# Optimization experiments

Measured on AMD Instinct MI355X. Metric: run time of the kernel, lower is better.

## Reference

```python
import jax, jax.numpy as jnp
import numpy as np

B, S, E, H, MAXLEN = 2, 2048, 1024, 16, 2048


def _level_indices(seq_len: int, base: int = 2) -> np.ndarray:
    """Vectorized version of get_level_index_weak over the full (target, source) grid.
    indices[t, s] = min(level, 2) for s < t, else 0. Runs in O(log S) passes."""
    tt = np.broadcast_to(np.arange(seq_len)[:, None], (seq_len, seq_len)).astype(np.int64).copy()
    ss = np.broadcast_to(np.arange(seq_len)[None, :], (seq_len, seq_len)).astype(np.int64).copy()
    res = np.zeros((seq_len, seq_len), np.int64)
    done = ~(ss < tt)  # only source < target positions get a level; rest stay 0
    while not done.all():
        l = np.floor(np.log2(np.maximum(tt, 1).astype(np.float64))).astype(np.int64)
        v = (np.int64(1) << l)
        hit = (~done) & (ss < v)
        res[hit] = l[hit] + 1
        done |= hit
        step = ~done
        tt[step] -= v[step]
        ss[step] -= v[step]
    return np.minimum(res, 2).astype(np.int32)


def setup_inputs() -> dict:
    key = jax.random.key(0)
    ks = jax.random.split(key, 10)
    sc = 0.02
    return {
        "x": jax.random.normal(ks[0], (B, S, E), dtype=jnp.float32),
        "attention_mask": jax.random.randint(ks[1], (B, S), 0, 2, dtype=jnp.int32),
        "level_indices": jnp.asarray(_level_indices(S, 2)),
        "Wq": jax.random.normal(ks[2], (E, E), dtype=jnp.float32) * sc,
        "bq": jnp.zeros((E,), jnp.float32),
        "Wk": jax.random.normal(ks[3], (E, E), dtype=jnp.float32) * sc,
        "bk": jnp.zeros((E,), jnp.float32),
        "Wv": jax.random.normal(ks[4], (E, E), dtype=jnp.float32) * sc,
        "bv": jnp.zeros((E,), jnp.float32),
        "hier": jax.random.normal(ks[5], (MAXLEN, H, 3), dtype=jnp.float32),
        "Wo": jax.random.normal(ks[6], (E, E), dtype=jnp.float32) * sc,
        "bo": jnp.zeros((E,), jnp.float32),
    }


def reference(x, attention_mask, level_indices, Wq, bq, Wk, bk, Wv, bv, hier, Wo, bo):
    b, s, e = x.shape
    h = hier.shape[1]
    dh = e // h
    # q/k are computed by the original module but never used; kept for fidelity (zero grads).
    q = x @ Wq.T + bq
    k = x @ Wk.T + bk
    v = (x @ Wv.T + bv).reshape(b, s, h, dh).transpose(0, 2, 1, 3)  # [B,H,S,Dh]
    lev = level_indices[:s, :s]  # [S,S] int, values in {0,1,2}
    # Faithful torch.gather semantics: weights[b,h,i,j] = hier[b, h, lev[i,j]]
    w3 = hier[:b]                      # [B,H,3]
    weights = w3[:, :, lev]            # [B,H,S,S]
    decay = jnp.power(jnp.float32(0.5), lev.astype(x.dtype))  # [S,S]
    weights = weights * decay
    weights = weights / (jnp.sum(weights, axis=-1, keepdims=True) + 1e-8)
    weights = jnp.where(attention_mask[:, None, None, :] == 0, jnp.float32(0.0), weights)
    out = jnp.einsum('bhij,bhjd->bhid', weights, v)  # [B,H,S,Dh]
    out = out.transpose(0, 2, 1, 3).reshape(b, s, e)
    return out @ Wo.T + bo
```

## Files before the change

### kernel.cpp

```cpp
#include <hip/hip_runtime.h>
#include <cstdint>
#include <cstddef>

constexpr int Sn = 2048;
constexpr int En = 1024;
constexpr int Bn = 2;
constexpr int Hn = 16;
constexpr int CHUNK = 32;
constexpr int NCH = Sn / CHUNK;
constexpr int Mtot = Bn * Sn;
constexpr int GCH = Mtot / CHUNK;

typedef __bf16 bf16x8 __attribute__((ext_vector_type(8)));
typedef float  f32x4  __attribute__((ext_vector_type(4)));

#define GLOBAL_AS(p) ((const __attribute__((address_space(1))) void*)(p))
#define LDS_AS(p)    ((__attribute__((address_space(3))) void*)(p))

__device__ __forceinline__ unsigned short f2bf(float f) {
    union { float f; uint32_t u; } v; v.f = f;
    const uint32_t u = v.u;
    return (unsigned short)((u + 0x7fffu + ((u >> 16) & 1u)) >> 16);
}
__device__ __forceinline__ float bf2f(unsigned short s) {
    union { uint32_t u; float f; } v; v.u = (uint32_t)s << 16; return v.f;
}

constexpr int XN = Bn * Sn * En;
constexpr int WN = En * En;

__global__ __launch_bounds__(256)
void cast3(const float* __restrict__ x, const float* __restrict__ Wv,
           const float* __restrict__ Wo, unsigned short* __restrict__ xb,
           unsigned short* __restrict__ Wvb, unsigned short* __restrict__ Wob)
{
    const int i = (blockIdx.x * 256 + threadIdx.x) * 4;
    const float* src; unsigned short* dst; int off;
    if (i < XN)           { src = x;  dst = xb;  off = i; }
    else if (i < XN + WN) { src = Wv; dst = Wvb; off = i - XN; }
    else                  { src = Wo; dst = Wob; off = i - XN - WN; }
    const float4 v = *(const float4*)(src + off);
    ushort4 o;
    o.x = f2bf(v.x); o.y = f2bf(v.y); o.z = f2bf(v.z); o.w = f2bf(v.w);
    *(ushort4*)(dst + off) = o;
}

template<bool APPLY_MASK, bool OUT_BF16, bool FUSE_CSUM>
__global__ __launch_bounds__(256, 4)
void gemm64(const unsigned short* __restrict__ A, const unsigned short* __restrict__ Bw,
            const float* __restrict__ bias, const int* __restrict__ mask,
            void* __restrict__ Cv, float* __restrict__ csum, int M, int N, int K)
{
    __shared__ __align__(16) unsigned short As[64 * 64];
    __shared__ __align__(16) unsigned short Bs[64 * 64];

    const int tid  = threadIdx.x;
    const int lane = tid & 63;
    const int wv   = tid >> 6;
    const int wr   = wv >> 1;
    const int wc   = wv & 1;
    const int id   = blockIdx.y * 16 + blockIdx.x;
    const int xcd  = id & 7;
    const int slot = id >> 3;
    const int by   = xcd * 8 + (slot >> 4);
    const int bx   = slot & 15;
    const int bm   = by * 64;
    const int bn   = bx * 64;
    const int m16  = lane & 15;
    const int kq   = lane >> 4;

    f32x4 acc[2][2] = {};

    const unsigned short* gA = A  + (size_t)(bm + 16 * wv + m16) * K + kq * 8;
    const unsigned short* gB = Bw + (size_t)(bn + 16 * wv + m16) * K + kq * 8;
    unsigned short* lA0 = &As[(wv * 2 + 0) * 512];
    unsigned short* lA1 = &As[(wv * 2 + 1) * 512];
    unsigned short* lB0 = &Bs[(wv * 2 + 0) * 512];
    unsigned short* lB1 = &Bs[(wv * 2 + 1) * 512];

#pragma unroll 1
    for (int k0 = 0; k0 < K; k0 += 64) {
        __syncthreads();
        __builtin_amdgcn_global_load_lds(GLOBAL_AS(gA + k0),      LDS_AS(lA0), 16, 0, 0);
        __builtin_amdgcn_global_load_lds(GLOBAL_AS(gA + k0 + 32), LDS_AS(lA1), 16, 0, 0);
        __builtin_amdgcn_global_load_lds(GLOBAL_AS(gB + k0),      LDS_AS(lB0), 16, 0, 0);
        __builtin_amdgcn_global_load_lds(GLOBAL_AS(gB + k0 + 32), LDS_AS(lB1), 16, 0, 0);
        __syncthreads();

        bf16x8 af[2][2], bfr[2][2];
#pragma unroll
        for (int i = 0; i < 2; ++i)
#pragma unroll
            for (int kh = 0; kh < 2; ++kh) {
                af[i][kh]  = *(const bf16x8*)&As[((2 * wr + i) * 2 + kh) * 512 + lane * 8];
                bfr[i][kh] = *(const bf16x8*)&Bs[((2 * wc + i) * 2 + kh) * 512 + lane * 8];
            }
#pragma unroll
        for (int kh = 0; kh < 2; ++kh)
#pragma unroll
            for (int i = 0; i < 2; ++i)
#pragma unroll
                for (int j = 0; j < 2; ++j)
                    acc[i][j] = __builtin_amdgcn_mfma_f32_16x16x32_bf16(af[i][kh], bfr[j][kh], acc[i][j], 0, 0, 0);
    }

    float colsum[2] = {0.0f, 0.0f};
#pragma unroll
    for (int i = 0; i < 2; ++i) {
        const int r0 = bm + wr * 32 + i * 16 + kq * 4;
#pragma unroll
        for (int j = 0; j < 2; ++j) {
            const int c0 = bn + wc * 32 + j * 16 + m16;
            const float bcol = bias[c0];
#pragma unroll
            for (int r = 0; r < 4; ++r) {
                const int row = r0 + r;
                float val = acc[i][j][r] + bcol;
                if (APPLY_MASK) val = (mask[row] == 0) ? 0.0f : val;
                if (FUSE_CSUM) colsum[j] += val;
                if (OUT_BF16)
                    ((unsigned short*)Cv)[(size_t)row * N + c0] = f2bf(val);
                else
                    ((float*)Cv)[(size_t)row * N + c0] = val;
            }
        }
    }

    if (FUSE_CSUM) {
        const int gc = 2 * by + wr;
#pragma unroll
        for (int j = 0; j < 2; ++j) {
            float s = colsum[j];
            s += __shfl_xor(s, 16, 64);
            s += __shfl_xor(s, 32, 64);
            if (kq == 0)
                csum[(size_t)gc * En + bn + wc * 32 + j * 16 + m16] = s;
        }
    }
}

__global__ __launch_bounds__(256)
void combine(const unsigned short* __restrict__ vm, const float* __restrict__ csum,
             const float* __restrict__ hier, unsigned short* __restrict__ opre)
{
    const int e = blockIdx.x * 256 + threadIdx.x;
    const int c = blockIdx.y;
    const int b = blockIdx.z;
    const int h = e >> 6;

    const float w0 = hier[((size_t)b * Hn + h) * 3 + 0];
    const float w1 = hier[((size_t)b * Hn + h) * 3 + 1] * 0.5f;
    const float w2 = hier[((size_t)b * Hn + h) * 3 + 2] * 0.25f;

    float run = 0.0f, T = 0.0f;
    const int g0 = b * NCH;
    for (int c2 = 0; c2 < NCH; ++c2) {
        const float v = csum[(size_t)(g0 + c2) * En + e];
        if (c2 < c) run += v;
        T += v;
    }

    float prev = 0.0f;
    const size_t base = ((size_t)b * Sn + c * CHUNK) * En + e;

    for (int t = 0; t < CHUNK; ++t) {
        const int i = c * CHUNK + t;
        const float cur = bf2f(vm[base + (size_t)t * En]);
        float num, Z;
        if (i & 1) {
            num = w2 * (run - prev) + w1 * prev + w0 * (T - run);
            Z = (float)(i - 1) * w2 + w1 + (float)(Sn - i) * w0 + 1e-8f;
        } else {
            num = w2 * run + w0 * (T - run);
            Z = (float)i * w2 + (float)(Sn - i) * w0 + 1e-8f;
        }
        opre[base + (size_t)t * En] = f2bf(num / Z);
        run += cur;
        prev = cur;
    }
}

extern "C" void kernel_launch(void* const* d_in, const int* in_sizes, int n_in,
                              void* d_out, int out_size, void* d_ws, size_t ws_size,
                              hipStream_t stream)
{
    const float* x    = (const float*)d_in[0];
    const int*   mask = (const int*)d_in[1];
    const float* Wv   = (const float*)d_in[7];
    const float* bv   = (const float*)d_in[8];
    const float* hier = (const float*)d_in[9];
    const float* Wo   = (const float*)d_in[10];
    const float* bo   = (const float*)d_in[11];
    float* out = (float*)d_out;

    const int M = Mtot, N = En, K = En;

    char* ws = (char*)d_ws;
    unsigned short* xb    = (unsigned short*)ws;  ws += (size_t)M * K * 2;
    unsigned short* Wvb   = (unsigned short*)ws;  ws += (size_t)N * K * 2;
    unsigned short* Wob   = (unsigned short*)ws;  ws += (size_t)N * K * 2;
    unsigned short* vmb   = (unsigned short*)ws;  ws += (size_t)M * N * 2;
    float*          csum  = (float*)ws;           ws += (size_t)GCH * En * 4;
    unsigned short* opreb = (unsigned short*)ws;  ws += (size_t)M * N * 2;

    dim3 threads(256);

    cast3<<<dim3((XN + 2 * WN) / 1024), threads, 0, stream>>>(x, Wv, Wo, xb, Wvb, Wob);

    dim3 gemm_grid(16, 64);

    gemm64<true, true, true><<<gemm_grid, threads, 0, stream>>>(xb, Wvb, bv, mask, vmb, csum, M, N, K);
    combine<<<dim3(En / 256, NCH, Bn), threads, 0, stream>>>(vmb, csum, hier, opreb);
    gemm64<false, false, false><<<gemm_grid, threads, 0, stream>>>(opreb, Wob, bo, nullptr, out, nullptr, M, N, K);
}
```

Before: 181.4 us.

## Pre-swizzle operands into MFMA fragment layout and drop LDS staging in GEMMs

The cast and combine kernels now write bf16 operands in a blocked layout that matches the MFMA 16x32 fragment order. The GEMM then loads fragments straight from global memory into registers with no LDS or barriers. The block tile grows to 128x64 with 4x2 accumulators per wave, and CHUNK doubles to 64 to match the new row tiling of the column sums. The cost is that operand reuse now relies on L2/cache instead of LDS, and the combine kernel's writes become scattered.

```diff
diff --git a/kernel.cpp b/kernel.cpp
--- a/kernel.cpp
+++ b/kernel.cpp
@@ -6,16 +6,14 @@
 constexpr int En = 1024;
 constexpr int Bn = 2;
 constexpr int Hn = 16;
-constexpr int CHUNK = 32;
+constexpr int CHUNK = 64;
 constexpr int NCH = Sn / CHUNK;
 constexpr int Mtot = Bn * Sn;
 constexpr int GCH = Mtot / CHUNK;
+constexpr int KB = En / 32;
 
 typedef __bf16 bf16x8 __attribute__((ext_vector_type(8)));
 typedef float  f32x4  __attribute__((ext_vector_type(4)));
-
-#define GLOBAL_AS(p) ((const __attribute__((address_space(1))) void*)(p))
-#define LDS_AS(p)    ((__attribute__((address_space(3))) void*)(p))
 
 __device__ __forceinline__ unsigned short f2bf(float f) {
     union { float f; uint32_t u; } v; v.f = f;
@@ -24,6 +22,11 @@
 }
 __device__ __forceinline__ float bf2f(unsigned short s) {
     union { uint32_t u; float f; } v; v.u = (uint32_t)s << 16; return v.f;
+}
+
+__device__ __forceinline__ size_t swz_idx(int r, int c, int kb ) {
+    const int blk = (r >> 4) * kb + (c >> 5);
+    return (size_t)blk * 512 + (((r & 15) + (((c >> 3) & 3) << 4)) << 3) + (c & 7);
 }
 
 constexpr int XN = Bn * Sn * En;
@@ -42,18 +45,16 @@
     const float4 v = *(const float4*)(src + off);
     ushort4 o;
     o.x = f2bf(v.x); o.y = f2bf(v.y); o.z = f2bf(v.z); o.w = f2bf(v.w);
-    *(ushort4*)(dst + off) = o;
+    const int r = off >> 10, c = off & 1023;
+    *(ushort4*)(dst + swz_idx(r, c, KB)) = o;
 }
 
 template<bool APPLY_MASK, bool OUT_BF16, bool FUSE_CSUM>
-__global__ __launch_bounds__(256, 4)
-void gemm64(const unsigned short* __restrict__ A, const unsigned short* __restrict__ Bw,
-            const float* __restrict__ bias, const int* __restrict__ mask,
-            void* __restrict__ Cv, float* __restrict__ csum, int M, int N, int K)
-{
-    __shared__ __align__(16) unsigned short As[64 * 64];
-    __shared__ __align__(16) unsigned short Bs[64 * 64];
-
+__global__ __launch_bounds__(256)
+void gemm_flat(const unsigned short* __restrict__ A, const unsigned short* __restrict__ Bw,
+               const float* __restrict__ bias, const int* __restrict__ mask,
+               void* __restrict__ Cv, float* __restrict__ csum)
+{
     const int tid  = threadIdx.x;
     const int lane = tid & 63;
     const int wv   = tid >> 6;
@@ -62,52 +63,42 @@
     const int id   = blockIdx.y * 16 + blockIdx.x;
     const int xcd  = id & 7;
     const int slot = id >> 3;
-    const int by   = xcd * 8 + (slot >> 4);
+    const int by   = xcd * 4 + (slot >> 4);
     const int bx   = slot & 15;
-    const int bm   = by * 64;
+    const int bm   = by * 128;
     const int bn   = bx * 64;
     const int m16  = lane & 15;
     const int kq   = lane >> 4;
 
-    f32x4 acc[2][2] = {};
-
-    const unsigned short* gA = A  + (size_t)(bm + 16 * wv + m16) * K + kq * 8;
-    const unsigned short* gB = Bw + (size_t)(bn + 16 * wv + m16) * K + kq * 8;
-    unsigned short* lA0 = &As[(wv * 2 + 0) * 512];
-    unsigned short* lA1 = &As[(wv * 2 + 1) * 512];
-    unsigned short* lB0 = &Bs[(wv * 2 + 0) * 512];
-    unsigned short* lB1 = &Bs[(wv * 2 + 1) * 512];
-
-#pragma unroll 1
-    for (int k0 = 0; k0 < K; k0 += 64) {
-        __syncthreads();
-        __builtin_amdgcn_global_load_lds(GLOBAL_AS(gA + k0),      LDS_AS(lA0), 16, 0, 0);
-        __builtin_amdgcn_global_load_lds(GLOBAL_AS(gA + k0 + 32), LDS_AS(lA1), 16, 0, 0);
-        __builtin_amdgcn_global_load_lds(GLOBAL_AS(gB + k0),      LDS_AS(lB0), 16, 0, 0);
-        __builtin_amdgcn_global_load_lds(GLOBAL_AS(gB + k0 + 32), LDS_AS(lB1), 16, 0, 0);
-        __syncthreads();
-
-        bf16x8 af[2][2], bfr[2][2];
-#pragma unroll
-        for (int i = 0; i < 2; ++i)
-#pragma unroll
-            for (int kh = 0; kh < 2; ++kh) {
-                af[i][kh]  = *(const bf16x8*)&As[((2 * wr + i) * 2 + kh) * 512 + lane * 8];
-                bfr[i][kh] = *(const bf16x8*)&Bs[((2 * wc + i) * 2 + kh) * 512 + lane * 8];
-            }
-#pragma unroll
-        for (int kh = 0; kh < 2; ++kh)
-#pragma unroll
-            for (int i = 0; i < 2; ++i)
-#pragma unroll
-                for (int j = 0; j < 2; ++j)
-                    acc[i][j] = __builtin_amdgcn_mfma_f32_16x16x32_bf16(af[i][kh], bfr[j][kh], acc[i][j], 0, 0, 0);
+    f32x4 acc[4][2] = {};
+
+    const int rb = by * 8 + wr * 4;
+    const int cb = bx * 4 + wc * 2;
+    const unsigned short* aBase = A  + (size_t)rb * KB * 512 + lane * 8;
+    const unsigned short* bBase = Bw + (size_t)cb * KB * 512 + lane * 8;
+
+#pragma unroll 4
+    for (int kc = 0; kc < KB; ++kc) {
+        bf16x8 af0 = *(const bf16x8*)(aBase + (size_t)(0 * KB + kc) * 512);
+        bf16x8 af1 = *(const bf16x8*)(aBase + (size_t)(1 * KB + kc) * 512);
+        bf16x8 af2 = *(const bf16x8*)(aBase + (size_t)(2 * KB + kc) * 512);
+        bf16x8 af3 = *(const bf16x8*)(aBase + (size_t)(3 * KB + kc) * 512);
+        bf16x8 bf0 = *(const bf16x8*)(bBase + (size_t)(0 * KB + kc) * 512);
+        bf16x8 bf1 = *(const bf16x8*)(bBase + (size_t)(1 * KB + kc) * 512);
+        acc[0][0] = __builtin_amdgcn_mfma_f32_16x16x32_bf16(af0, bf0, acc[0][0], 0, 0, 0);
+        acc[0][1] = __builtin_amdgcn_mfma_f32_16x16x32_bf16(af0, bf1, acc[0][1], 0, 0, 0);
+        acc[1][0] = __builtin_amdgcn_mfma_f32_16x16x32_bf16(af1, bf0, acc[1][0], 0, 0, 0);
+        acc[1][1] = __builtin_amdgcn_mfma_f32_16x16x32_bf16(af1, bf1, acc[1][1], 0, 0, 0);
+        acc[2][0] = __builtin_amdgcn_mfma_f32_16x16x32_bf16(af2, bf0, acc[2][0], 0, 0, 0);
+        acc[2][1] = __builtin_amdgcn_mfma_f32_16x16x32_bf16(af2, bf1, acc[2][1], 0, 0, 0);
+        acc[3][0] = __builtin_amdgcn_mfma_f32_16x16x32_bf16(af3, bf0, acc[3][0], 0, 0, 0);
+        acc[3][1] = __builtin_amdgcn_mfma_f32_16x16x32_bf16(af3, bf1, acc[3][1], 0, 0, 0);
     }
 
     float colsum[2] = {0.0f, 0.0f};
 #pragma unroll
-    for (int i = 0; i < 2; ++i) {
-        const int r0 = bm + wr * 32 + i * 16 + kq * 4;
+    for (int i = 0; i < 4; ++i) {
+        const int r0 = bm + wr * 64 + i * 16 + kq * 4;
 #pragma unroll
         for (int j = 0; j < 2; ++j) {
             const int c0 = bn + wc * 32 + j * 16 + m16;
@@ -119,9 +110,9 @@
                 if (APPLY_MASK) val = (mask[row] == 0) ? 0.0f : val;
                 if (FUSE_CSUM) colsum[j] += val;
                 if (OUT_BF16)
-                    ((unsigned short*)Cv)[(size_t)row * N + c0] = f2bf(val);
+                    ((unsigned short*)Cv)[(size_t)row * En + c0] = f2bf(val);
                 else
-                    ((float*)Cv)[(size_t)row * N + c0] = val;
+                    ((float*)Cv)[(size_t)row * En + c0] = val;
             }
         }
     }
@@ -159,6 +150,10 @@
         if (c2 < c) run += v;
         T += v;
     }
+
+    const int ecol  = (e >> 5);
+    const int elane = ((e >> 3) & 3) << 4;
+    const int epos  = e & 7;
 
     float prev = 0.0f;
     const size_t base = ((size_t)b * Sn + c * CHUNK) * En + e;
@@ -174,7 +169,10 @@
             num = w2 * run + w0 * (T - run);
             Z = (float)i * w2 + (float)(Sn - i) * w0 + 1e-8f;
         }
-        opre[base + (size_t)t * En] = f2bf(num / Z);
+        const int gi = b * Sn + i;
+        const size_t di = (size_t)((gi >> 4) * KB + ecol) * 512
+                        + ((((gi & 15) + elane)) << 3) + epos;
+        opre[di] = f2bf(num / Z);
         run += cur;
         prev = cur;
     }
@@ -193,23 +191,21 @@
     const float* bo   = (const float*)d_in[11];
     float* out = (float*)d_out;
 
-    const int M = Mtot, N = En, K = En;
-
     char* ws = (char*)d_ws;
-    unsigned short* xb    = (unsigned short*)ws;  ws += (size_t)M * K * 2;
-    unsigned short* Wvb   = (unsigned short*)ws;  ws += (size_t)N * K * 2;
-    unsigned short* Wob   = (unsigned short*)ws;  ws += (size_t)N * K * 2;
-    unsigned short* vmb   = (unsigned short*)ws;  ws += (size_t)M * N * 2;
+    unsigned short* xb    = (unsigned short*)ws;  ws += (size_t)Mtot * En * 2;
+    unsigned short* Wvb   = (unsigned short*)ws;  ws += (size_t)En * En * 2;
+    unsigned short* Wob   = (unsigned short*)ws;  ws += (size_t)En * En * 2;
+    unsigned short* vmb   = (unsigned short*)ws;  ws += (size_t)Mtot * En * 2;
     float*          csum  = (float*)ws;           ws += (size_t)GCH * En * 4;
-    unsigned short* opreb = (unsigned short*)ws;  ws += (size_t)M * N * 2;
+    unsigned short* opreb = (unsigned short*)ws;  ws += (size_t)Mtot * En * 2;
 
     dim3 threads(256);
 
     cast3<<<dim3((XN + 2 * WN) / 1024), threads, 0, stream>>>(x, Wv, Wo, xb, Wvb, Wob);
 
-    dim3 gemm_grid(16, 64);
-
-    gemm64<true, true, true><<<gemm_grid, threads, 0, stream>>>(xb, Wvb, bv, mask, vmb, csum, M, N, K);
+    dim3 gemm_grid(16, 32);
+
+    gemm_flat<true, true, true><<<gemm_grid, threads, 0, stream>>>(xb, Wvb, bv, mask, vmb, csum);
     combine<<<dim3(En / 256, NCH, Bn), threads, 0, stream>>>(vmb, csum, hier, opreb);
-    gemm64<false, false, false><<<gemm_grid, threads, 0, stream>>>(opreb, Wob, bo, nullptr, out, nullptr, M, N, K);
-}
+    gemm_flat<false, false, false><<<gemm_grid, threads, 0, stream>>>(opreb, Wob, bo, nullptr, out, nullptr);
+}
```

Measured after the change: 180.3 us. Within noise of the previous version (-0.6%).
